# Kernel optimization log

Hardware: AMD Instinct MI355X
Metric: run time of the kernel (lower is better)

## Reference

```python
import jax, jax.numpy as jnp
import numpy as np

DIM = 1024
B, L = 8, 2048
ACT = DIM // 4          # sparse_ratio 0.25
HID = DIM // 4          # LowRankFF reduction 4
EPS = 1e-6
K, DILATION = 5, 1
PAD = (K - 1) * DILATION // 2


def setup_inputs() -> dict:
    key = jax.random.key(0)
    ks = jax.random.split(key, 16)
    s = lambda fan_in: 1.0 / np.sqrt(fan_in)
    return {
        "x": jax.random.normal(ks[0], (B, L, DIM), jnp.float32),
        "norm_w": jnp.ones((DIM,), jnp.float32),
        "dw_w": jax.random.normal(ks[1], (DIM, 1, K), jnp.float32) * s(K),
        "dw_b": jax.random.normal(ks[2], (DIM,), jnp.float32) * s(K),
        "pw_w": jax.random.normal(ks[3], (DIM, DIM), jnp.float32) * s(DIM),
        "pw_b": jax.random.normal(ks[4], (DIM,), jnp.float32) * s(DIM),
        "alpha": jnp.full((ACT,), 0.9, jnp.float32),
        "beta": jnp.full((ACT,), 0.1, jnp.float32),
        "W1_w": jax.random.normal(ks[5], (DIM, DIM), jnp.float32) * s(DIM),
        "W1_b": jax.random.normal(ks[6], (DIM,), jnp.float32) * s(DIM),
        "W2_w": jax.random.normal(ks[7], (DIM, DIM), jnp.float32) * s(DIM),
        "W2_b": jax.random.normal(ks[8], (DIM,), jnp.float32) * s(DIM),
        "down_w": jax.random.normal(ks[9], (HID, DIM), jnp.float32) * s(DIM),
        "down_b": jax.random.normal(ks[10], (HID,), jnp.float32) * s(DIM),
        "up_w": jax.random.normal(ks[11], (DIM, HID), jnp.float32) * s(HID),
        "up_b": jax.random.normal(ks[12], (DIM,), jnpp := jnp.float32) * s(HID),
    }


def reference(x, norm_w, dw_w, dw_b, pw_w, pw_b, alpha, beta,
              W1_w, W1_b, W2_w, W2_b, down_w, down_b, up_w, up_b):
    residual = x
    # RMSNorm
    rms = jnp.sqrt(jnp.mean(x * x, axis=-1, keepdims=True) + EPS)
    xn = norm_w * (x / rms)                              # [B,L,D]
    # depthwise conv (groups=DIM), NCH layout; same-length output
    xc = jax.lax.conv_general_dilated(
        xn.transpose(0, 2, 1), dw_w,
        window_strides=(1,), padding=[(PAD, PAD)],
        rhs_dilation=(DILATION,), feature_group_count=DIM,
        dimension_numbers=("NCH", "OIH", "NCH")) + dw_b[None, :, None]
    xc = xc.transpose(0, 2, 1)                           # [B,L,D]
    # pointwise conv == dense linear over channels
    x_conv = jnp.einsum("bld,od->blo", xc, pw_w) + pw_b
    # sparse shift-gate recurrence on FIRST ACT channels (faithful to source)
    x_act = xn[:, :, :ACT]                               # [B,L,A]

    def step(h, xt):                                     # h,xt: [B,A]
        h = alpha * h + beta * xt
        return h, h

    _, hs = jax.lax.scan(step, jnp.zeros((B, ACT), xn.dtype),
                         x_act.transpose(1, 0, 2))       # hs: [L,B,A]
    x_rec = jnp.concatenate([hs.transpose(1, 0, 2), xn[:, :, ACT:]], axis=-1)
    # gated fusion
    y = x_conv + x_rec
    y = y + jax.nn.sigmoid(y @ W1_w.T + W1_b) * jnp.tanh(y @ W2_w.T + W2_b)
    # low-rank FF (exact gelu, matching torch F.gelu default)
    y = y + (jax.nn.gelu(y @ down_w.T + down_b, approximate=False) @ up_w.T + up_b)
    return y + residual
```

## Files before the change

### kernel.cpp

```cpp
#include <hip/hip_runtime.h>
#include <math.h>

#define DIMC 1024
#define BB   8
#define LL   2048
#define ACTC 256
#define HIDC 256
#define EPSV 1e-6f
#define MROWS (BB * LL)
#define NCHUNK 32
#define LC     64

typedef __bf16 bf16x8 __attribute__((ext_vector_type(8)));
typedef float  f32x4  __attribute__((ext_vector_type(4)));

__device__ __forceinline__ unsigned short f2bf(float f) {
    union { float f; unsigned int u; } v; v.f = f;
    unsigned int u = v.u + 0x7fffu + ((v.u >> 16) & 1u);
    return (unsigned short)(u >> 16);
}
__device__ __forceinline__ float bf2f(unsigned short s) {
    union { float f; unsigned int u; } v; v.u = ((unsigned int)s) << 16;
    return v.f;
}
__device__ __forceinline__ float fast_sigmoid(float x) {
    return 1.0f / (1.0f + __expf(-x));
}
__device__ __forceinline__ float fast_tanh(float x) {
    float ax = fabsf(x);
    float t = 1.0f - 2.0f / (__expf(2.0f * ax) + 1.0f);
    return copysignf(t, x);
}

__global__ void k_convert5(const float* __restrict__ s0, const float* __restrict__ s1,
                           const float* __restrict__ s2, const float* __restrict__ s3,
                           const float* __restrict__ s4,
                           unsigned short* __restrict__ d0, unsigned short* __restrict__ d1,
                           unsigned short* __restrict__ d2, unsigned short* __restrict__ d3,
                           unsigned short* __restrict__ d4) {
    int i = blockIdx.x * blockDim.x + threadIdx.x;
    if (i < 1048576)            d0[i]           = f2bf(s0[i]);
    else if (i < 2097152)       d1[i - 1048576] = f2bf(s1[i - 1048576]);
    else if (i < 3145728)       d2[i - 2097152] = f2bf(s2[i - 2097152]);
    else if (i < 3407872)       d3[i - 3145728] = f2bf(s3[i - 3145728]);
    else if (i < 3670016)       d4[i - 3407872] = f2bf(s4[i - 3407872]);
}

__global__ __launch_bounds__(256) void k_rmsnorm(const float* __restrict__ x,
                                                 const float* __restrict__ w,
                                                 unsigned short* __restrict__ xnb) {
    int m = blockIdx.x;
    int t = threadIdx.x;
    float4 v = ((const float4*)(x + (size_t)m * DIMC))[t];
    float ss = v.x*v.x + v.y*v.y + v.z*v.z + v.w*v.w;
#pragma unroll
    for (int off = 32; off > 0; off >>= 1) ss += __shfl_down(ss, off, 64);
    __shared__ float sred[4];
    if ((t & 63) == 0) sred[t >> 6] = ss;
    __syncthreads();
    float tot = sred[0] + sred[1] + sred[2] + sred[3];
    float rinv = 1.0f / sqrtf(tot * (1.0f / DIMC) + EPSV);
    float4 wv = ((const float4*)w)[t];
    uint2 o;
    o.x = (unsigned)f2bf(wv.x * v.x * rinv) | ((unsigned)f2bf(wv.y * v.y * rinv) << 16);
    o.y = (unsigned)f2bf(wv.z * v.z * rinv) | ((unsigned)f2bf(wv.w * v.w * rinv) << 16);
    ((uint2*)(xnb + (size_t)m * DIMC))[t] = o;
}

__global__ __launch_bounds__(256) void k_dwconv(const unsigned short* __restrict__ xnb,
                                                const float* __restrict__ dww,
                                                const float* __restrict__ dwb,
                                                unsigned short* __restrict__ xc) {
    int m = blockIdx.x;
    int l = m & (LL - 1);
    int t = threadIdx.x;
    int c0 = t * 4;
    float wgt[4][5];
#pragma unroll
    for (int j = 0; j < 4; ++j)
#pragma unroll
        for (int k = 0; k < 5; ++k) wgt[j][k] = dww[(c0 + j) * 5 + k];
    float4 bv = ((const float4*)dwb)[t];
    float acc[4] = {bv.x, bv.y, bv.z, bv.w};
#pragma unroll
    for (int k = 0; k < 5; ++k) {
        int ll = l + k - 2;
        if (ll < 0 || ll >= LL) continue;
        uint2 rv = ((const uint2*)(xnb + (size_t)(m + k - 2) * DIMC))[t];
        acc[0] += bf2f((unsigned short)(rv.x & 0xffff)) * wgt[0][k];
        acc[1] += bf2f((unsigned short)(rv.x >> 16))    * wgt[1][k];
        acc[2] += bf2f((unsigned short)(rv.y & 0xffff)) * wgt[2][k];
        acc[3] += bf2f((unsigned short)(rv.y >> 16))    * wgt[3][k];
    }
    uint2 o;
    o.x = (unsigned)f2bf(acc[0]) | ((unsigned)f2bf(acc[1]) << 16);
    o.y = (unsigned)f2bf(acc[2]) | ((unsigned)f2bf(acc[3]) << 16);
    ((uint2*)(xc + (size_t)m * DIMC))[t] = o;
}

__global__ __launch_bounds__(256) void k_scan_a(const unsigned short* __restrict__ xnb,
                                                const float* __restrict__ alpha,
                                                const float* __restrict__ beta,
                                                float* __restrict__ F) {
    int blk = blockIdx.x;
    int b = blk >> 5, k = blk & (NCHUNK - 1);
    int c = threadIdx.x;
    float a = alpha[c], bt = beta[c];
    const unsigned short* p = xnb + ((size_t)(b * LL + k * LC)) * DIMC + c;
    float h = 0.0f;
    for (int l = 0; l < LC; ++l) h = a * h + bt * bf2f(p[(size_t)l * DIMC]);
    F[(size_t)blk * ACTC + c] = h;
}
__global__ __launch_bounds__(256) void k_scan_b(const float* __restrict__ alpha,
                                                const float* __restrict__ F,
                                                float* __restrict__ Cv) {
    int b = blockIdx.x;
    int c = threadIdx.x;
    float a = alpha[c];
    float aL = a;
#pragma unroll
    for (int i = 0; i < 6; ++i) aL *= aL;
    float T = 0.0f;
    for (int k = 0; k < NCHUNK; ++k) {
        size_t idx = ((size_t)b * NCHUNK + k) * ACTC + c;
        Cv[idx] = T;
        T = F[idx] + aL * T;
    }
}
__global__ __launch_bounds__(256) void k_scan_c(const unsigned short* __restrict__ xnb,
                                                const float* __restrict__ alpha,
                                                const float* __restrict__ beta,
                                                const float* __restrict__ Cv,
                                                unsigned short* __restrict__ hs) {
    int blk = blockIdx.x;
    int b = blk >> 5, k = blk & (NCHUNK - 1);
    int c = threadIdx.x;
    float a = alpha[c], bt = beta[c];
    const unsigned short* p = xnb + ((size_t)(b * LL + k * LC)) * DIMC + c;
    unsigned short*       q = hs  + ((size_t)(b * LL + k * LC)) * ACTC + c;
    float h = Cv[(size_t)blk * ACTC + c];
    for (int l = 0; l < LC; ++l) {
        h = a * h + bt * bf2f(p[(size_t)l * DIMC]);
        q[(size_t)l * ACTC] = f2bf(h);
    }
}

#define TM 128
#define TN 128
#define BK 64

#define GLOAD_LDS(gp, lp) \
    __builtin_amdgcn_global_load_lds((const __attribute__((address_space(1))) unsigned int*)(gp), \
                                     (__attribute__((address_space(3))) unsigned int*)(lp), 16, 0, 0)

template<int MODE>
__global__ __launch_bounds__(256, (MODE == 1) ? 2 : 4) void k_gemm(
        const unsigned short* __restrict__ A,
        const unsigned short* __restrict__ B0,
        const unsigned short* __restrict__ B1,
        const float* __restrict__ bias0,
        const float* __restrict__ bias1,
        const unsigned short* __restrict__ add0,
        const unsigned short* __restrict__ add1,
        const float* __restrict__ addf,
        float* __restrict__ outf,
        unsigned short* __restrict__ outb,
        int M, int N, int K)
{
    constexpr int LDSB = (MODE == 1) ? 49152 : 32768;
    __shared__ __align__(16) char lds[LDSB];
    unsigned short* sA  = (unsigned short*)lds;
    unsigned short* sB0 = (unsigned short*)(lds + 16384);
    unsigned short* sB1 = (unsigned short*)(lds + 32768);

    int nx = gridDim.x;
    int bid = blockIdx.y * nx + blockIdx.x;
    int xcd = bid & 7, s = bid >> 3;
    int colt = s % nx, rowgrp = s / nx;
    int m0 = (rowgrp * 8 + xcd) * TM;
    int n0 = colt * TN;

    int t = threadIdx.x;
    int w = t >> 6, lane = t & 63;
    int wm = (w >> 1) * 64, wn = (w & 1) * 64;
    int quad = lane >> 4, lm = lane & 15;
    int lm7 = lm & 7;

    f32x4 zero = {0.f, 0.f, 0.f, 0.f};
    f32x4 acc0[4][4];
    f32x4 acc1[(MODE == 1) ? 4 : 1][(MODE == 1) ? 4 : 1];
#pragma unroll
    for (int i = 0; i < 4; ++i)
#pragma unroll
        for (int j = 0; j < 4; ++j) acc0[i][j] = zero;
    if constexpr (MODE == 1) {
#pragma unroll
        for (int i = 0; i < 4; ++i)
#pragma unroll
            for (int j = 0; j < 4; ++j) acc1[i][j] = zero;
    }

    for (int k0 = 0; k0 < K; k0 += BK) {
        __syncthreads();
#pragma unroll
        for (int c = 0; c < 4; ++c) {
            int i = t + c * 256;
            int r = i >> 3;
            int sc = ((i & 7) ^ (r & 7)) << 3;
            GLOAD_LDS(A  + (size_t)(m0 + r) * K + k0 + sc, sA  + i * 8);
            GLOAD_LDS(B0 + (size_t)(n0 + r) * K + k0 + sc, sB0 + i * 8);
            if constexpr (MODE == 1)
                GLOAD_LDS(B1 + (size_t)(n0 + r) * K + k0 + sc, sB1 + i * 8);
        }
        __syncthreads();

#pragma unroll
        for (int ks = 0; ks < BK; ks += 32) {
            int cgb = ks >> 3;
            bf16x8 af[4], b0f[4];
#pragma unroll
            for (int i = 0; i < 4; ++i) {
                int sg = ((cgb + quad) ^ lm7) << 3;
                af[i]  = *(const bf16x8*)(sA  + (wm + i * 16 + lm) * BK + sg);
                b0f[i] = *(const bf16x8*)(sB0 + (wn + i * 16 + lm) * BK + sg);
            }
            if constexpr (MODE == 1) {
                bf16x8 b1f[4];
#pragma unroll
                for (int i = 0; i < 4; ++i)
                    b1f[i] = *(const bf16x8*)(sB1 + (wn + i * 16 + lm) * BK + (((cgb + quad) ^ lm7) << 3));
#pragma unroll
                for (int mi = 0; mi < 4; ++mi)
#pragma unroll
                    for (int ni = 0; ni < 4; ++ni) {
                        acc0[mi][ni] = __builtin_amdgcn_mfma_f32_16x16x32_bf16(af[mi], b0f[ni], acc0[mi][ni], 0, 0, 0);
                        acc1[mi][ni] = __builtin_amdgcn_mfma_f32_16x16x32_bf16(af[mi], b1f[ni], acc1[mi][ni], 0, 0, 0);
                    }
            } else {
#pragma unroll
                for (int mi = 0; mi < 4; ++mi)
#pragma unroll
                    for (int ni = 0; ni < 4; ++ni)
                        acc0[mi][ni] = __builtin_amdgcn_mfma_f32_16x16x32_bf16(af[mi], b0f[ni], acc0[mi][ni], 0, 0, 0);
            }
        }
    }

    __syncthreads();
    if constexpr (MODE == 3) {
        float* sO = (float*)lds;
#pragma unroll
        for (int half = 0; half < 2; ++half) {
            if (wm == half * 64) {
#pragma unroll
                for (int mi = 0; mi < 4; ++mi) {
#pragma unroll
                    for (int ni = 0; ni < 4; ++ni) {
                        int nl = wn + ni * 16 + lm;
                        float bn = bias0[n0 + nl];
#pragma unroll
                        for (int j = 0; j < 4; ++j) {
                            int mloc = mi * 16 + quad * 4 + j;
                            sO[mloc * TN + nl] = acc0[mi][ni][j] + bn;
                        }
                    }
                }
            }
            __syncthreads();
#pragma unroll
            for (int c = 0; c < 8; ++c) {
                int i = t + c * 256;
                int r = i >> 5, c4 = (i & 31) << 2;
                int m = m0 + half * 64 + r, n = n0 + c4;
                float4 v  = *(float4*)(sO + r * TN + c4);
                uint2  ab = *(const uint2*)(add0 + (size_t)m * N + n);
                float4 xf = *(const float4*)(addf + (size_t)m * N + n);
                float4 o;
                o.x = v.x + bf2f((unsigned short)(ab.x & 0xffff)) + xf.x;
                o.y = v.y + bf2f((unsigned short)(ab.x >> 16))    + xf.y;
                o.z = v.z + bf2f((unsigned short)(ab.y & 0xffff)) + xf.z;
                o.w = v.w + bf2f((unsigned short)(ab.y >> 16))    + xf.w;
                *(float4*)(outf + (size_t)m * N + n) = o;
            }
            __syncthreads();
        }
    } else {
        unsigned short* sO = (unsigned short*)lds;
#pragma unroll
        for (int mi = 0; mi < 4; ++mi) {
#pragma unroll
            for (int ni = 0; ni < 4; ++ni) {
                int nl = wn + ni * 16 + lm;
                int n  = n0 + nl;
                float bn = bias0[n];
                float bn1 = (MODE == 1) ? bias1[n] : 0.0f;
#pragma unroll
                for (int j = 0; j < 4; ++j) {
                    int ml = wm + mi * 16 + quad * 4 + j;
                    float v = acc0[mi][ni][j];
                    float r;
                    if constexpr (MODE == 0) {
                        r = v + bn;
                    } else if constexpr (MODE == 1) {
                        float u1 = v + bn;
                        float u2 = acc1[mi][ni][j] + bn1;
                        r = fast_sigmoid(u1) * fast_tanh(u2);
                    } else {
                        float u = v + bn;
                        r = 0.5f * u * (1.0f + erff(u * 0.70710678118654752f));
                    }
                    sO[ml * TN + nl] = f2bf(r);
                }
            }
        }
        __syncthreads();
#pragma unroll
        for (int c = 0; c < 8; ++c) {
            int i = t + c * 256;
            int r = i >> 4, c8 = (i & 15) << 3;
            int m = m0 + r, n = n0 + c8;
            uint4 g = *(uint4*)(sO + r * TN + c8);
            if constexpr (MODE == 2) {
                *(uint4*)(outb + (size_t)m * N + n) = g;
            } else {
                uint4 av;
                if constexpr (MODE == 0) {
                    av = (n0 < ACTC) ? *(const uint4*)(add0 + (size_t)m * ACTC + n)
                                     : *(const uint4*)(add1 + (size_t)m * DIMC + n);
                } else {
                    av = *(const uint4*)(add0 + (size_t)m * N + n);
                }
                unsigned* gp = (unsigned*)&g;
                unsigned* ap = (unsigned*)&av;
                uint4 o;
                unsigned* op = (unsigned*)&o;
#pragma unroll
                for (int q = 0; q < 4; ++q) {
                    float lo = bf2f((unsigned short)(gp[q] & 0xffff)) + bf2f((unsigned short)(ap[q] & 0xffff));
                    float hi = bf2f((unsigned short)(gp[q] >> 16))    + bf2f((unsigned short)(ap[q] >> 16));
                    op[q] = (unsigned)f2bf(lo) | ((unsigned)f2bf(hi) << 16);
                }
                *(uint4*)(outb + (size_t)m * N + n) = o;
            }
        }
    }
}

template<int MODE>
__global__ __launch_bounds__(256, (MODE == 1) ? 3 : 4) void k_gemm64(
        const unsigned short* __restrict__ A,
        const unsigned short* __restrict__ B0,
        const unsigned short* __restrict__ B1,
        const float* __restrict__ bias0,
        const float* __restrict__ bias1,
        const unsigned short* __restrict__ add0,
        unsigned short* __restrict__ outb,
        int M, int N, int K)
{
    constexpr int LDSB = (MODE == 1) ? 32768 : 24576;
    __shared__ __align__(16) char lds[LDSB];
    unsigned short* sA  = (unsigned short*)lds;
    unsigned short* sB0 = (unsigned short*)(lds + 16384);
    unsigned short* sB1 = (unsigned short*)(lds + 24576);

    int nx = gridDim.x;
    int bid = blockIdx.y * nx + blockIdx.x;
    int xcd = bid & 7, s = bid >> 3;
    int colt = s % nx, rowgrp = s / nx;
    int m0 = (rowgrp * 8 + xcd) * TM;
    int n0 = colt * 64;

    int t = threadIdx.x;
    int w = t >> 6, lane = t & 63;
    int wm = (w >> 1) * 64, wn = (w & 1) * 32;
    int quad = lane >> 4, lm = lane & 15;
    int lm7 = lm & 7;

    f32x4 zero = {0.f, 0.f, 0.f, 0.f};
    f32x4 acc0[4][2];
    f32x4 acc1[(MODE == 1) ? 4 : 1][(MODE == 1) ? 2 : 1];
#pragma unroll
    for (int i = 0; i < 4; ++i)
#pragma unroll
        for (int j = 0; j < 2; ++j) acc0[i][j] = zero;
    if constexpr (MODE == 1) {
#pragma unroll
        for (int i = 0; i < 4; ++i)
#pragma unroll
            for (int j = 0; j < 2; ++j) acc1[i][j] = zero;
    }

    for (int k0 = 0; k0 < K; k0 += BK) {
        __syncthreads();
#pragma unroll
        for (int c = 0; c < 4; ++c) {
            int i = t + c * 256;
            int r = i >> 3;
            int sc = ((i & 7) ^ (r & 7)) << 3;
            GLOAD_LDS(A + (size_t)(m0 + r) * K + k0 + sc, sA + i * 8);
        }
#pragma unroll
        for (int c = 0; c < 2; ++c) {
            int i = t + c * 256;
            int r = i >> 3;
            int sc = ((i & 7) ^ (r & 7)) << 3;
            GLOAD_LDS(B0 + (size_t)(n0 + r) * K + k0 + sc, sB0 + i * 8);
            if constexpr (MODE == 1)
                GLOAD_LDS(B1 + (size_t)(n0 + r) * K + k0 + sc, sB1 + i * 8);
        }
        __syncthreads();

#pragma unroll
        for (int ks = 0; ks < BK; ks += 32) {
            int cgb = ks >> 3;
            int sg = ((cgb + quad) ^ lm7) << 3;
            bf16x8 af[4], b0f[2];
#pragma unroll
            for (int i = 0; i < 4; ++i)
                af[i] = *(const bf16x8*)(sA + (wm + i * 16 + lm) * BK + sg);
#pragma unroll
            for (int i = 0; i < 2; ++i)
                b0f[i] = *(const bf16x8*)(sB0 + (wn + i * 16 + lm) * BK + sg);
            if constexpr (MODE == 1) {
                bf16x8 b1f[2];
#pragma unroll
                for (int i = 0; i < 2; ++i)
                    b1f[i] = *(const bf16x8*)(sB1 + (wn + i * 16 + lm) * BK + sg);
#pragma unroll
                for (int mi = 0; mi < 4; ++mi)
#pragma unroll
                    for (int ni = 0; ni < 2; ++ni) {
                        acc0[mi][ni] = __builtin_amdgcn_mfma_f32_16x16x32_bf16(af[mi], b0f[ni], acc0[mi][ni], 0, 0, 0);
                        acc1[mi][ni] = __builtin_amdgcn_mfma_f32_16x16x32_bf16(af[mi], b1f[ni], acc1[mi][ni], 0, 0, 0);
                    }
            } else {
#pragma unroll
                for (int mi = 0; mi < 4; ++mi)
#pragma unroll
                    for (int ni = 0; ni < 2; ++ni)
                        acc0[mi][ni] = __builtin_amdgcn_mfma_f32_16x16x32_bf16(af[mi], b0f[ni], acc0[mi][ni], 0, 0, 0);
            }
        }
    }

    __syncthreads();
    unsigned short* sO = (unsigned short*)lds;
#pragma unroll
    for (int mi = 0; mi < 4; ++mi) {
#pragma unroll
        for (int ni = 0; ni < 2; ++ni) {
            int nl = wn + ni * 16 + lm;
            int n  = n0 + nl;
            float bn = bias0[n];
            float bn1 = (MODE == 1) ? bias1[n] : 0.0f;
#pragma unroll
            for (int j = 0; j < 4; ++j) {
                int ml = wm + mi * 16 + quad * 4 + j;
                float r;
                if constexpr (MODE == 1) {
                    float u1 = acc0[mi][ni][j] + bn;
                    float u2 = acc1[mi][ni][j] + bn1;
                    r = fast_sigmoid(u1) * fast_tanh(u2);
                } else {
                    float u = acc0[mi][ni][j] + bn;
                    r = 0.5f * u * (1.0f + erff(u * 0.70710678118654752f));
                }
                sO[ml * 64 + nl] = f2bf(r);
            }
        }
    }
    __syncthreads();
#pragma unroll
    for (int c = 0; c < 4; ++c) {
        int i = t + c * 256;
        int r = i >> 3, c8 = (i & 7) << 3;
        int m = m0 + r, n = n0 + c8;
        uint4 g = *(uint4*)(sO + r * 64 + c8);
        if constexpr (MODE == 2) {
            *(uint4*)(outb + (size_t)m * N + n) = g;
        } else {
            uint4 av = *(const uint4*)(add0 + (size_t)m * N + n);
            unsigned* gp = (unsigned*)&g;
            unsigned* ap = (unsigned*)&av;
            uint4 o;
            unsigned* op = (unsigned*)&o;
#pragma unroll
            for (int q = 0; q < 4; ++q) {
                float lo = bf2f((unsigned short)(gp[q] & 0xffff)) + bf2f((unsigned short)(ap[q] & 0xffff));
                float hi = bf2f((unsigned short)(gp[q] >> 16))    + bf2f((unsigned short)(ap[q] >> 16));
                op[q] = (unsigned)f2bf(lo) | ((unsigned)f2bf(hi) << 16);
            }
            *(uint4*)(outb + (size_t)m * N + n) = o;
        }
    }
}

extern "C" void kernel_launch(void* const* d_in, const int* in_sizes, int n_in,
                              void* d_out, int out_size, void* d_ws, size_t ws_size,
                              hipStream_t stream) {
    (void)in_sizes; (void)n_in; (void)out_size; (void)ws_size;
    const float* x      = (const float*)d_in[0];
    const float* norm_w = (const float*)d_in[1];
    const float* dw_w   = (const float*)d_in[2];
    const float* dw_b   = (const float*)d_in[3];
    const float* pw_w   = (const float*)d_in[4];
    const float* pw_b   = (const float*)d_in[5];
    const float* alpha  = (const float*)d_in[6];
    const float* beta   = (const float*)d_in[7];
    const float* W1_w   = (const float*)d_in[8];
    const float* W1_b   = (const float*)d_in[9];
    const float* W2_w   = (const float*)d_in[10];
    const float* W2_b   = (const float*)d_in[11];
    const float* down_w = (const float*)d_in[12];
    const float* down_b = (const float*)d_in[13];
    const float* up_w   = (const float*)d_in[14];
    const float* up_b   = (const float*)d_in[15];

    char* ws = (char*)d_ws;
    unsigned short* xnb  = (unsigned short*)(ws);
    unsigned short* xc   = (unsigned short*)(ws + 33554432ull);
    unsigned short* hs   = (unsigned short*)(ws + 67108864ull);
    unsigned short* y1b  = (unsigned short*)(ws + 75497472ull);
    unsigned short* y2b  = (unsigned short*)(ws + 109051904ull);
    unsigned short* gact = (unsigned short*)(ws + 142606336ull);
    unsigned short* wpw  = (unsigned short*)(ws + 150994944ull);
    unsigned short* w1b  = wpw + 1048576;
    unsigned short* w2b  = w1b + 1048576;
    unsigned short* wdn  = w2b + 1048576;
    unsigned short* wup  = wdn + 262144;
    float*          Fb   = (float*)(ws + 159383552ull);
    float*          Cb   = (float*)(ws + 159383552ull + 262144ull);

    k_convert5<<<14336, 256, 0, stream>>>(pw_w, W1_w, W2_w, down_w, up_w,
                                          wpw, w1b, w2b, wdn, wup);

    k_rmsnorm<<<MROWS, 256, 0, stream>>>(x, norm_w, xnb);
    k_dwconv <<<MROWS, 256, 0, stream>>>(xnb, dw_w, dw_b, xc);

    k_scan_a<<<BB * NCHUNK, ACTC, 0, stream>>>(xnb, alpha, beta, Fb);
    k_scan_b<<<BB, ACTC, 0, stream>>>(alpha, Fb, Cb);
    k_scan_c<<<BB * NCHUNK, ACTC, 0, stream>>>(xnb, alpha, beta, Cb, hs);

    dim3 g1(DIMC / TN, MROWS / TM);
    dim3 g1b(DIMC / 64, MROWS / TM);
    dim3 g2b(HIDC / 64, MROWS / TM);
    k_gemm<0><<<g1, 256, 0, stream>>>(xc, wpw, nullptr, pw_b, nullptr, hs, xnb, nullptr, nullptr, y1b, MROWS, DIMC, DIMC);
    k_gemm64<1><<<g1b, 256, 0, stream>>>(y1b, w1b, w2b, W1_b, W2_b, y1b, y2b, MROWS, DIMC, DIMC);
    k_gemm64<2><<<g2b, 256, 0, stream>>>(y2b, wdn, nullptr, down_b, nullptr, nullptr, gact, MROWS, HIDC, DIMC);
    k_gemm<3><<<g1, 256, 0, stream>>>(gact, wup, nullptr, up_b, nullptr, y2b, nullptr, x, (float*)d_out, nullptr, MROWS, DIMC, HIDC);
}
```

Before: 379.8 us.

## Fuse RMSNorm with dwconv, interleave W1/W2 into one GEMM, drop scan_b

```diff
diff --git a/kernel.cpp b/kernel.cpp
--- a/kernel.cpp
+++ b/kernel.cpp
@@ -35,67 +35,91 @@
 __global__ void k_convert5(const float* __restrict__ s0, const float* __restrict__ s1,
                            const float* __restrict__ s2, const float* __restrict__ s3,
                            const float* __restrict__ s4,
-                           unsigned short* __restrict__ d0, unsigned short* __restrict__ d1,
-                           unsigned short* __restrict__ d2, unsigned short* __restrict__ d3,
-                           unsigned short* __restrict__ d4) {
+                           unsigned short* __restrict__ d0, unsigned short* __restrict__ d12,
+                           unsigned short* __restrict__ d3, unsigned short* __restrict__ d4) {
     int i = blockIdx.x * blockDim.x + threadIdx.x;
-    if (i < 1048576)            d0[i]           = f2bf(s0[i]);
-    else if (i < 2097152)       d1[i - 1048576] = f2bf(s1[i - 1048576]);
-    else if (i < 3145728)       d2[i - 2097152] = f2bf(s2[i - 2097152]);
-    else if (i < 3407872)       d3[i - 3145728] = f2bf(s3[i - 3145728]);
-    else if (i < 3670016)       d4[i - 3407872] = f2bf(s4[i - 3407872]);
-}
-
-__global__ __launch_bounds__(256) void k_rmsnorm(const float* __restrict__ x,
-                                                 const float* __restrict__ w,
-                                                 unsigned short* __restrict__ xnb) {
-    int m = blockIdx.x;
+    if (i < 1048576) {
+        d0[i] = f2bf(s0[i]);
+    } else if (i < 2097152) {
+        int j = i - 1048576; int n = j >> 10, kk = j & 1023;
+        d12[(size_t)(n * 2) * 1024 + kk] = f2bf(s1[j]);
+    } else if (i < 3145728) {
+        int j = i - 2097152; int n = j >> 10, kk = j & 1023;
+        d12[(size_t)(n * 2 + 1) * 1024 + kk] = f2bf(s2[j]);
+    } else if (i < 3407872) {
+        d3[i - 3145728] = f2bf(s3[i - 3145728]);
+    } else if (i < 3670016) {
+        d4[i - 3407872] = f2bf(s4[i - 3407872]);
+    }
+}
+
+__global__ __launch_bounds__(256, 2) void k_normconv(
+        const float* __restrict__ x, const float* __restrict__ w,
+        const float* __restrict__ dww, const float* __restrict__ dwb,
+        unsigned short* __restrict__ xnb, unsigned short* __restrict__ xc) {
+    __shared__ unsigned short sxn[36 * 1024];
+    int blk = blockIdx.x;
+    int b = blk >> 6, s = blk & 63;
+    int l0 = s * 32;
     int t = threadIdx.x;
-    float4 v = ((const float4*)(x + (size_t)m * DIMC))[t];
-    float ss = v.x*v.x + v.y*v.y + v.z*v.z + v.w*v.w;
-#pragma unroll
-    for (int off = 32; off > 0; off >>= 1) ss += __shfl_down(ss, off, 64);
-    __shared__ float sred[4];
-    if ((t & 63) == 0) sred[t >> 6] = ss;
+    int lane = t & 63, wid = t >> 6;
+
+    float4 nw[4];
+#pragma unroll
+    for (int j = 0; j < 4; ++j) nw[j] = ((const float4*)w)[j * 64 + lane];
+
+    for (int rr = wid; rr < 36; rr += 4) {
+        int l = l0 - 2 + rr;
+        bool inr = (l >= 0 && l < LL);
+        float4 v[4];
+#pragma unroll
+        for (int j = 0; j < 4; ++j) { v[j].x = 0.f; v[j].y = 0.f; v[j].z = 0.f; v[j].w = 0.f; }
+        if (inr) {
+            const float4* xp = (const float4*)(x + ((size_t)b * LL + l) * DIMC);
+#pragma unroll
+            for (int j = 0; j < 4; ++j) v[j] = xp[j * 64 + lane];
+        }
+        float ss = 0.f;
+#pragma unroll
+        for (int j = 0; j < 4; ++j)
+            ss += v[j].x * v[j].x + v[j].y * v[j].y + v[j].z * v[j].z + v[j].w * v[j].w;
+#pragma unroll
+        for (int off = 1; off < 64; off <<= 1) ss += __shfl_xor(ss, off, 64);
+        float rinv = 1.0f / sqrtf(ss * (1.0f / DIMC) + EPSV);
+#pragma unroll
+        for (int j = 0; j < 4; ++j) {
+            uint2 o;
+            o.x = (unsigned)f2bf(nw[j].x * v[j].x * rinv) | ((unsigned)f2bf(nw[j].y * v[j].y * rinv) << 16);
+            o.y = (unsigned)f2bf(nw[j].z * v[j].z * rinv) | ((unsigned)f2bf(nw[j].w * v[j].w * rinv) << 16);
+            ((uint2*)(sxn + rr * 1024))[j * 64 + lane] = o;
+            if (inr && rr >= 2 && rr < 34)
+                ((uint2*)(xnb + ((size_t)b * LL + l) * DIMC))[j * 64 + lane] = o;
+        }
+    }
     __syncthreads();
-    float tot = sred[0] + sred[1] + sred[2] + sred[3];
-    float rinv = 1.0f / sqrtf(tot * (1.0f / DIMC) + EPSV);
-    float4 wv = ((const float4*)w)[t];
-    uint2 o;
-    o.x = (unsigned)f2bf(wv.x * v.x * rinv) | ((unsigned)f2bf(wv.y * v.y * rinv) << 16);
-    o.y = (unsigned)f2bf(wv.z * v.z * rinv) | ((unsigned)f2bf(wv.w * v.w * rinv) << 16);
-    ((uint2*)(xnb + (size_t)m * DIMC))[t] = o;
-}
-
-__global__ __launch_bounds__(256) void k_dwconv(const unsigned short* __restrict__ xnb,
-                                                const float* __restrict__ dww,
-                                                const float* __restrict__ dwb,
-                                                unsigned short* __restrict__ xc) {
-    int m = blockIdx.x;
-    int l = m & (LL - 1);
-    int t = threadIdx.x;
+
+    float wgt[4][5];
     int c0 = t * 4;
-    float wgt[4][5];
 #pragma unroll
     for (int j = 0; j < 4; ++j)
 #pragma unroll
         for (int k = 0; k < 5; ++k) wgt[j][k] = dww[(c0 + j) * 5 + k];
     float4 bv = ((const float4*)dwb)[t];
-    float acc[4] = {bv.x, bv.y, bv.z, bv.w};
-#pragma unroll
-    for (int k = 0; k < 5; ++k) {
-        int ll = l + k - 2;
-        if (ll < 0 || ll >= LL) continue;
-        uint2 rv = ((const uint2*)(xnb + (size_t)(m + k - 2) * DIMC))[t];
-        acc[0] += bf2f((unsigned short)(rv.x & 0xffff)) * wgt[0][k];
-        acc[1] += bf2f((unsigned short)(rv.x >> 16))    * wgt[1][k];
-        acc[2] += bf2f((unsigned short)(rv.y & 0xffff)) * wgt[2][k];
-        acc[3] += bf2f((unsigned short)(rv.y >> 16))    * wgt[3][k];
-    }
-    uint2 o;
-    o.x = (unsigned)f2bf(acc[0]) | ((unsigned)f2bf(acc[1]) << 16);
-    o.y = (unsigned)f2bf(acc[2]) | ((unsigned)f2bf(acc[3]) << 16);
-    ((uint2*)(xc + (size_t)m * DIMC))[t] = o;
+    for (int r = 0; r < 32; ++r) {
+        float acc[4] = {bv.x, bv.y, bv.z, bv.w};
+#pragma unroll
+        for (int k = 0; k < 5; ++k) {
+            uint2 rv = ((const uint2*)(sxn + (r + k) * 1024))[t];
+            acc[0] += bf2f((unsigned short)(rv.x & 0xffff)) * wgt[0][k];
+            acc[1] += bf2f((unsigned short)(rv.x >> 16))    * wgt[1][k];
+            acc[2] += bf2f((unsigned short)(rv.y & 0xffff)) * wgt[2][k];
+            acc[3] += bf2f((unsigned short)(rv.y >> 16))    * wgt[3][k];
+        }
+        uint2 o;
+        o.x = (unsigned)f2bf(acc[0]) | ((unsigned)f2bf(acc[1]) << 16);
+        o.y = (unsigned)f2bf(acc[2]) | ((unsigned)f2bf(acc[3]) << 16);
+        ((uint2*)(xc + ((size_t)b * LL + l0 + r) * DIMC))[t] = o;
+    }
 }
 
 __global__ __launch_bounds__(256) void k_scan_a(const unsigned short* __restrict__ xnb,
@@ -111,34 +135,24 @@
     for (int l = 0; l < LC; ++l) h = a * h + bt * bf2f(p[(size_t)l * DIMC]);
     F[(size_t)blk * ACTC + c] = h;
 }
-__global__ __launch_bounds__(256) void k_scan_b(const float* __restrict__ alpha,
-                                                const float* __restrict__ F,
-                                                float* __restrict__ Cv) {
-    int b = blockIdx.x;
-    int c = threadIdx.x;
-    float a = alpha[c];
-    float aL = a;
-#pragma unroll
-    for (int i = 0; i < 6; ++i) aL *= aL;
-    float T = 0.0f;
-    for (int k = 0; k < NCHUNK; ++k) {
-        size_t idx = ((size_t)b * NCHUNK + k) * ACTC + c;
-        Cv[idx] = T;
-        T = F[idx] + aL * T;
-    }
-}
 __global__ __launch_bounds__(256) void k_scan_c(const unsigned short* __restrict__ xnb,
                                                 const float* __restrict__ alpha,
                                                 const float* __restrict__ beta,
-                                                const float* __restrict__ Cv,
+                                                const float* __restrict__ F,
                                                 unsigned short* __restrict__ hs) {
     int blk = blockIdx.x;
     int b = blk >> 5, k = blk & (NCHUNK - 1);
     int c = threadIdx.x;
     float a = alpha[c], bt = beta[c];
+    float aL = a;
+#pragma unroll
+    for (int i = 0; i < 6; ++i) aL *= aL;
+    float T = 0.0f;
+    for (int j = 0; j < k; ++j)
+        T = F[((size_t)b * NCHUNK + j) * ACTC + c] + aL * T;
     const unsigned short* p = xnb + ((size_t)(b * LL + k * LC)) * DIMC + c;
     unsigned short*       q = hs  + ((size_t)(b * LL + k * LC)) * ACTC + c;
-    float h = Cv[(size_t)blk * ACTC + c];
+    float h = T;
     for (int l = 0; l < LC; ++l) {
         h = a * h + bt * bf2f(p[(size_t)l * DIMC]);
         q[(size_t)l * ACTC] = f2bf(h);
@@ -154,10 +168,9 @@
                                      (__attribute__((address_space(3))) unsigned int*)(lp), 16, 0, 0)
 
 template<int MODE>
-__global__ __launch_bounds__(256, (MODE == 1) ? 2 : 4) void k_gemm(
+__global__ __launch_bounds__(256, 4) void k_gemm(
         const unsigned short* __restrict__ A,
         const unsigned short* __restrict__ B0,
-        const unsigned short* __restrict__ B1,
         const float* __restrict__ bias0,
         const float* __restrict__ bias1,
         const unsigned short* __restrict__ add0,
@@ -167,11 +180,9 @@
         unsigned short* __restrict__ outb,
         int M, int N, int K)
 {
-    constexpr int LDSB = (MODE == 1) ? 49152 : 32768;
-    __shared__ __align__(16) char lds[LDSB];
+    __shared__ __align__(16) char lds[32768];
     unsigned short* sA  = (unsigned short*)lds;
     unsigned short* sB0 = (unsigned short*)(lds + 16384);
-    unsigned short* sB1 = (unsigned short*)(lds + 32768);
 
     int nx = gridDim.x;
     int bid = blockIdx.y * nx + blockIdx.x;
@@ -188,17 +199,10 @@
 
     f32x4 zero = {0.f, 0.f, 0.f, 0.f};
     f32x4 acc0[4][4];
-    f32x4 acc1[(MODE == 1) ? 4 : 1][(MODE == 1) ? 4 : 1];
 #pragma unroll
     for (int i = 0; i < 4; ++i)
 #pragma unroll
         for (int j = 0; j < 4; ++j) acc0[i][j] = zero;
-    if constexpr (MODE == 1) {
-#pragma unroll
-        for (int i = 0; i < 4; ++i)
-#pragma unroll
-            for (int j = 0; j < 4; ++j) acc1[i][j] = zero;
-    }
 
     for (int k0 = 0; k0 < K; k0 += BK) {
         __syncthreads();
@@ -209,8 +213,6 @@
             int sc = ((i & 7) ^ (r & 7)) << 3;
             GLOAD_LDS(A  + (size_t)(m0 + r) * K + k0 + sc, sA  + i * 8);
             GLOAD_LDS(B0 + (size_t)(n0 + r) * K + k0 + sc, sB0 + i * 8);
-            if constexpr (MODE == 1)
-                GLOAD_LDS(B1 + (size_t)(n0 + r) * K + k0 + sc, sB1 + i * 8);
         }
         __syncthreads();
 
@@ -224,25 +226,11 @@
                 af[i]  = *(const bf16x8*)(sA  + (wm + i * 16 + lm) * BK + sg);
                 b0f[i] = *(const bf16x8*)(sB0 + (wn + i * 16 + lm) * BK + sg);
             }
-            if constexpr (MODE == 1) {
-                bf16x8 b1f[4];
-#pragma unroll
-                for (int i = 0; i < 4; ++i)
-                    b1f[i] = *(const bf16x8*)(sB1 + (wn + i * 16 + lm) * BK + (((cgb + quad) ^ lm7) << 3));
-#pragma unroll
-                for (int mi = 0; mi < 4; ++mi)
-#pragma unroll
-                    for (int ni = 0; ni < 4; ++ni) {
-                        acc0[mi][ni] = __builtin_amdgcn_mfma_f32_16x16x32_bf16(af[mi], b0f[ni], acc0[mi][ni], 0, 0, 0);
-                        acc1[mi][ni] = __builtin_amdgcn_mfma_f32_16x16x32_bf16(af[mi], b1f[ni], acc1[mi][ni], 0, 0, 0);
-                    }
-            } else {
-#pragma unroll
-                for (int mi = 0; mi < 4; ++mi)
-#pragma unroll
-                    for (int ni = 0; ni < 4; ++ni)
-                        acc0[mi][ni] = __builtin_amdgcn_mfma_f32_16x16x32_bf16(af[mi], b0f[ni], acc0[mi][ni], 0, 0, 0);
-            }
+#pragma unroll
+            for (int mi = 0; mi < 4; ++mi)
+#pragma unroll
+                for (int ni = 0; ni < 4; ++ni)
+                    acc0[mi][ni] = __builtin_amdgcn_mfma_f32_16x16x32_bf16(af[mi], b0f[ni], acc0[mi][ni], 0, 0, 0);
         }
     }
 
@@ -284,6 +272,46 @@
             }
             __syncthreads();
         }
+    } else if constexpr (MODE == 4) {
+        unsigned short* sO = (unsigned short*)lds;
+#pragma unroll
+        for (int mi = 0; mi < 4; ++mi) {
+#pragma unroll
+            for (int ni = 0; ni < 4; ++ni) {
+                int nl = wn + ni * 16 + lm;
+                int ng = n0 + nl;
+                float bn = (nl & 1) ? bias1[ng >> 1] : bias0[ng >> 1];
+#pragma unroll
+                for (int j = 0; j < 4; ++j) {
+                    int ml = wm + mi * 16 + quad * 4 + j;
+                    float u  = acc0[mi][ni][j] + bn;
+                    float uo = __shfl_xor(u, 1, 64);
+                    float ue = (nl & 1) ? uo : u;
+                    float ut = (nl & 1) ? u  : uo;
+                    float r = fast_sigmoid(ue) * fast_tanh(ut);
+                    if (!(nl & 1)) sO[ml * 64 + (nl >> 1)] = f2bf(r);
+                }
+            }
+        }
+        __syncthreads();
+#pragma unroll
+        for (int c = 0; c < 4; ++c) {
+            int i = t + c * 256;
+            int r = i >> 3, c8 = (i & 7) << 3;
+            int m = m0 + r, n = (n0 >> 1) + c8;
+            uint4 g  = *(uint4*)(sO + r * 64 + c8);
+            uint4 av = *(const uint4*)(add0 + (size_t)m * DIMC + n);
+            unsigned* gp = (unsigned*)&g;
+            unsigned* ap = (unsigned*)&av;
+            uint4 o; unsigned* op = (unsigned*)&o;
+#pragma unroll
+            for (int q = 0; q < 4; ++q) {
+                float lo = bf2f((unsigned short)(gp[q] & 0xffff)) + bf2f((unsigned short)(ap[q] & 0xffff));
+                float hi = bf2f((unsigned short)(gp[q] >> 16))    + bf2f((unsigned short)(ap[q] >> 16));
+                op[q] = (unsigned)f2bf(lo) | ((unsigned)f2bf(hi) << 16);
+            }
+            *(uint4*)(outb + (size_t)m * DIMC + n) = o;
+        }
     } else {
         unsigned short* sO = (unsigned short*)lds;
 #pragma unroll
@@ -293,7 +321,6 @@
                 int nl = wn + ni * 16 + lm;
                 int n  = n0 + nl;
                 float bn = bias0[n];
-                float bn1 = (MODE == 1) ? bias1[n] : 0.0f;
 #pragma unroll
                 for (int j = 0; j < 4; ++j) {
                     int ml = wm + mi * 16 + quad * 4 + j;
@@ -301,10 +328,6 @@
                     float r;
                     if constexpr (MODE == 0) {
                         r = v + bn;
-                    } else if constexpr (MODE == 1) {
-                        float u1 = v + bn;
-                        float u2 = acc1[mi][ni][j] + bn1;
-                        r = fast_sigmoid(u1) * fast_tanh(u2);
                     } else {
                         float u = v + bn;
                         r = 0.5f * u * (1.0f + erff(u * 0.70710678118654752f));
@@ -323,13 +346,8 @@
             if constexpr (MODE == 2) {
                 *(uint4*)(outb + (size_t)m * N + n) = g;
             } else {
-                uint4 av;
-                if constexpr (MODE == 0) {
-                    av = (n0 < ACTC) ? *(const uint4*)(add0 + (size_t)m * ACTC + n)
-                                     : *(const uint4*)(add1 + (size_t)m * DIMC + n);
-                } else {
-                    av = *(const uint4*)(add0 + (size_t)m * N + n);
-                }
+                uint4 av = (n0 < ACTC) ? *(const uint4*)(add0 + (size_t)m * ACTC + n)
+                                       : *(const uint4*)(add1 + (size_t)m * DIMC + n);
                 unsigned* gp = (unsigned*)&g;
                 unsigned* ap = (unsigned*)&av;
                 uint4 o;
@@ -347,21 +365,16 @@
 }
 
 template<int MODE>
-__global__ __launch_bounds__(256, (MODE == 1) ? 3 : 4) void k_gemm64(
+__global__ __launch_bounds__(256, 4) void k_gemm64(
         const unsigned short* __restrict__ A,
         const unsigned short* __restrict__ B0,
-        const unsigned short* __restrict__ B1,
         const float* __restrict__ bias0,
-        const float* __restrict__ bias1,
-        const unsigned short* __restrict__ add0,
         unsigned short* __restrict__ outb,
         int M, int N, int K)
 {
-    constexpr int LDSB = (MODE == 1) ? 32768 : 24576;
-    __shared__ __align__(16) char lds[LDSB];
+    __shared__ __align__(16) char lds[24576];
     unsigned short* sA  = (unsigned short*)lds;
     unsigned short* sB0 = (unsigned short*)(lds + 16384);
-    unsigned short* sB1 = (unsigned short*)(lds + 24576);
 
     int nx = gridDim.x;
     int bid = blockIdx.y * nx + blockIdx.x;
@@ -378,17 +391,10 @@
 
     f32x4 zero = {0.f, 0.f, 0.f, 0.f};
     f32x4 acc0[4][2];
-    f32x4 acc1[(MODE == 1) ? 4 : 1][(MODE == 1) ? 2 : 1];
 #pragma unroll
     for (int i = 0; i < 4; ++i)
 #pragma unroll
         for (int j = 0; j < 2; ++j) acc0[i][j] = zero;
-    if constexpr (MODE == 1) {
-#pragma unroll
-        for (int i = 0; i < 4; ++i)
-#pragma unroll
-            for (int j = 0; j < 2; ++j) acc1[i][j] = zero;
-    }
 
     for (int k0 = 0; k0 < K; k0 += BK) {
         __syncthreads();
@@ -405,8 +411,6 @@
             int r = i >> 3;
             int sc = ((i & 7) ^ (r & 7)) << 3;
             GLOAD_LDS(B0 + (size_t)(n0 + r) * K + k0 + sc, sB0 + i * 8);
-            if constexpr (MODE == 1)
-                GLOAD_LDS(B1 + (size_t)(n0 + r) * K + k0 + sc, sB1 + i * 8);
         }
         __syncthreads();
 
@@ -421,25 +425,11 @@
 #pragma unroll
             for (int i = 0; i < 2; ++i)
                 b0f[i] = *(const bf16x8*)(sB0 + (wn + i * 16 + lm) * BK + sg);
-            if constexpr (MODE == 1) {
-                bf16x8 b1f[2];
-#pragma unroll
-                for (int i = 0; i < 2; ++i)
-                    b1f[i] = *(const bf16x8*)(sB1 + (wn + i * 16 + lm) * BK + sg);
-#pragma unroll
-                for (int mi = 0; mi < 4; ++mi)
-#pragma unroll
-                    for (int ni = 0; ni < 2; ++ni) {
-                        acc0[mi][ni] = __builtin_amdgcn_mfma_f32_16x16x32_bf16(af[mi], b0f[ni], acc0[mi][ni], 0, 0, 0);
-                        acc1[mi][ni] = __builtin_amdgcn_mfma_f32_16x16x32_bf16(af[mi], b1f[ni], acc1[mi][ni], 0, 0, 0);
-                    }
-            } else {
-#pragma unroll
-                for (int mi = 0; mi < 4; ++mi)
-#pragma unroll
-                    for (int ni = 0; ni < 2; ++ni)
-                        acc0[mi][ni] = __builtin_amdgcn_mfma_f32_16x16x32_bf16(af[mi], b0f[ni], acc0[mi][ni], 0, 0, 0);
-            }
+#pragma unroll
+            for (int mi = 0; mi < 4; ++mi)
+#pragma unroll
+                for (int ni = 0; ni < 2; ++ni)
+                    acc0[mi][ni] = __builtin_amdgcn_mfma_f32_16x16x32_bf16(af[mi], b0f[ni], acc0[mi][ni], 0, 0, 0);
         }
     }
 
@@ -452,19 +442,11 @@
             int nl = wn + ni * 16 + lm;
             int n  = n0 + nl;
             float bn = bias0[n];
-            float bn1 = (MODE == 1) ? bias1[n] : 0.0f;
 #pragma unroll
             for (int j = 0; j < 4; ++j) {
                 int ml = wm + mi * 16 + quad * 4 + j;
-                float r;
-                if constexpr (MODE == 1) {
-                    float u1 = acc0[mi][ni][j] + bn;
-                    float u2 = acc1[mi][ni][j] + bn1;
-                    r = fast_sigmoid(u1) * fast_tanh(u2);
-                } else {
-                    float u = acc0[mi][ni][j] + bn;
-                    r = 0.5f * u * (1.0f + erff(u * 0.70710678118654752f));
-                }
+                float u = acc0[mi][ni][j] + bn;
+                float r = 0.5f * u * (1.0f + erff(u * 0.70710678118654752f));
                 sO[ml * 64 + nl] = f2bf(r);
             }
         }
@@ -476,22 +458,7 @@
         int r = i >> 3, c8 = (i & 7) << 3;
         int m = m0 + r, n = n0 + c8;
         uint4 g = *(uint4*)(sO + r * 64 + c8);
-        if constexpr (MODE == 2) {
-            *(uint4*)(outb + (size_t)m * N + n) = g;
-        } else {
-            uint4 av = *(const uint4*)(add0 + (size_t)m * N + n);
-            unsigned* gp = (unsigned*)&g;
-            unsigned* ap = (unsigned*)&av;
-            uint4 o;
-            unsigned* op = (unsigned*)&o;
-#pragma unroll
-            for (int q = 0; q < 4; ++q) {
-                float lo = bf2f((unsigned short)(gp[q] & 0xffff)) + bf2f((unsigned short)(ap[q] & 0xffff));
-                float hi = bf2f((unsigned short)(gp[q] >> 16))    + bf2f((unsigned short)(ap[q] >> 16));
-                op[q] = (unsigned)f2bf(lo) | ((unsigned)f2bf(hi) << 16);
-            }
-            *(uint4*)(outb + (size_t)m * N + n) = o;
-        }
+        *(uint4*)(outb + (size_t)m * N + n) = g;
     }
 }
 
@@ -524,28 +491,24 @@
     unsigned short* y2b  = (unsigned short*)(ws + 109051904ull);
     unsigned short* gact = (unsigned short*)(ws + 142606336ull);
     unsigned short* wpw  = (unsigned short*)(ws + 150994944ull);
-    unsigned short* w1b  = wpw + 1048576;
-    unsigned short* w2b  = w1b + 1048576;
-    unsigned short* wdn  = w2b + 1048576;
+    unsigned short* w12  = wpw + 1048576;
+    unsigned short* wdn  = wpw + 3145728;
     unsigned short* wup  = wdn + 262144;
     float*          Fb   = (float*)(ws + 159383552ull);
-    float*          Cb   = (float*)(ws + 159383552ull + 262144ull);
 
     k_convert5<<<14336, 256, 0, stream>>>(pw_w, W1_w, W2_w, down_w, up_w,
-                                          wpw, w1b, w2b, wdn, wup);
-
-    k_rmsnorm<<<MROWS, 256, 0, stream>>>(x, norm_w, xnb);
-    k_dwconv <<<MROWS, 256, 0, stream>>>(xnb, dw_w, dw_b, xc);
+                                          wpw, w12, wdn, wup);
+
+    k_normconv<<<BB * 64, 256, 0, stream>>>(x, norm_w, dw_w, dw_b, xnb, xc);
 
     k_scan_a<<<BB * NCHUNK, ACTC, 0, stream>>>(xnb, alpha, beta, Fb);
-    k_scan_b<<<BB, ACTC, 0, stream>>>(alpha, Fb, Cb);
-    k_scan_c<<<BB * NCHUNK, ACTC, 0, stream>>>(xnb, alpha, beta, Cb, hs);
-
-    dim3 g1(DIMC / TN, MROWS / TM);
-    dim3 g1b(DIMC / 64, MROWS / TM);
-    dim3 g2b(HIDC / 64, MROWS / TM);
-    k_gemm<0><<<g1, 256, 0, stream>>>(xc, wpw, nullptr, pw_b, nullptr, hs, xnb, nullptr, nullptr, y1b, MROWS, DIMC, DIMC);
-    k_gemm64<1><<<g1b, 256, 0, stream>>>(y1b, w1b, w2b, W1_b, W2_b, y1b, y2b, MROWS, DIMC, DIMC);
-    k_gemm64<2><<<g2b, 256, 0, stream>>>(y2b, wdn, nullptr, down_b, nullptr, nullptr, gact, MROWS, HIDC, DIMC);
-    k_gemm<3><<<g1, 256, 0, stream>>>(gact, wup, nullptr, up_b, nullptr, y2b, nullptr, x, (float*)d_out, nullptr, MROWS, DIMC, HIDC);
-}
+    k_scan_c<<<BB * NCHUNK, ACTC, 0, stream>>>(xnb, alpha, beta, Fb, hs);
+
+    dim3 g0(DIMC / TN, MROWS / TM);
+    dim3 g1(2 * DIMC / TN, MROWS / TM);
+    dim3 g2(HIDC / 64, MROWS / TM);
+    k_gemm<0><<<g0, 256, 0, stream>>>(xc, wpw, pw_b, nullptr, hs, xnb, nullptr, nullptr, y1b, MROWS, DIMC, DIMC);
+    k_gemm<4><<<g1, 256, 0, stream>>>(y1b, w12, W1_b, W2_b, y1b, nullptr, nullptr, nullptr, y2b, MROWS, 2 * DIMC, DIMC);
+    k_gemm64<2><<<g2, 256, 0, stream>>>(y2b, wdn, down_b, gact, MROWS, HIDC, DIMC);
+    k_gemm<3><<<g0, 256, 0, stream>>>(gact, wup, up_b, nullptr, y2b, nullptr, x, (float*)d_out, nullptr, MROWS, DIMC, HIDC);
+}
```

Result: no change. 372.6 us (-1.9%).
